# Kernel tuning notes

Hardware: AMD Instinct MI355X
Metric: run time of the kernel (lower is better)

The kernel has to match this reference:

```python
import jax, jax.numpy as jnp
import numpy as np

C = 8          # n_features
D = 256        # grid side
N = 1_000_000  # query points
K = 27         # kernel**3 neighborhood
OUTPUT_SCALE = 1.0


def _linear_params(key, fin, fout):
    kw, kb = jax.random.split(key)
    s = 1.0 / np.sqrt(fin)
    W = jax.random.uniform(kw, (fin, fout), jnp.float32, -s, s)
    b = jax.random.uniform(kb, (fout,), jnp.float32, -s, s)
    return W, b


def setup_inputs() -> dict:
    key = jax.random.key(0)
    ks = jax.random.split(key, 10)
    points = jax.random.uniform(ks[0], (N, 3), jnp.float32, 0.0, float(D - 1))
    grid = jax.random.normal(ks[1], (1, C, D, D, D), dtype=jnp.float32)
    Wc, bc = _linear_params(ks[2], K * C, C)
    W1, b1 = _linear_params(ks[3], 2 * C, 32)
    W2, b2 = _linear_params(ks[4], C + 32, 16)
    W3, b3 = _linear_params(ks[5], C + 16, 8)
    W4, b4 = _linear_params(ks[6], C + 8, C)
    Ws, bs = _linear_params(ks[7], C, 1)
    Wo, bo = _linear_params(ks[8], C, 1)
    return dict(points=points, grid=grid, Wc=Wc, bc=bc, W1=W1, b1=b1,
                W2=W2, b2=b2, W3=W3, b3=b3, W4=W4, b4=b4,
                Ws=Ws, bs=bs, Wo=Wo, bo=bo)


def _layernorm(z):
    # elementwise_affine=False, eps=1e-5, over last dim
    m = jnp.mean(z, axis=-1, keepdims=True)
    v = jnp.var(z, axis=-1, keepdims=True)
    return (z - m) * jax.lax.rsqrt(v + 1e-5)


def reference(points, grid, Wc, bc, W1, b1, W2, b2, W3, b3, W4, b4, Ws, bs, Wo, bo):
    act = jnp.tanh  # config.RENDERER.activation = torch.nn.Tanh()
    pad = 1  # kernel // 2
    # ReplicationPad3d on (1,C,D,H,W)
    g = jnp.pad(grid[0], ((0, 0), (pad, pad), (pad, pad), (pad, pad)), mode='edge')  # (C, D+2, D+2, D+2)
    pts = points + pad
    idx = jnp.floor(pts).astype(jnp.int32)  # (N,3)
    # 27-neighborhood offsets in loop order i,j,k in range(-1,2)
    r = jnp.arange(-1, 2)
    off = jnp.stack(jnp.meshgrid(r, r, r, indexing='ij'), axis=-1).reshape(K, 3)
    nb = idx[:, None, :] + off[None].astype(jnp.int32)  # (N,27,3)
    feat = g[:, nb[..., 0], nb[..., 1], nb[..., 2]]  # (C, N, 27)
    feat = jnp.transpose(feat, (1, 2, 0))            # (N, 27, C) point-major, neighbor, channel
    cen = g[:, idx[:, 0], idx[:, 1], idx[:, 2]].T    # (N, C)
    # use_count_renderer: normalize last channel (count) by global max
    max_count = jnp.maximum(jnp.max(feat[..., -1]), jnp.max(cen[:, -1])) + 1e-9
    feat = jnp.concatenate([feat[..., :-1], feat[..., -1:] / max_count], axis=-1)
    cen = jnp.concatenate([cen[:, :-1], cen[:, -1:] / max_count], axis=-1)
    x = feat.reshape(feat.shape[0], K * C)  # matches torch contiguous view (neighbor-then-channel)
    # DenseNet-style tiny MLP chain (Dropout2d is identity in eval)
    ctx = act(_layernorm(x @ Wc + bc))
    h = act(jnp.concatenate([cen, ctx], axis=1) @ W1 + b1)
    h = act(jnp.concatenate([cen, h], axis=1) @ W2 + b2)
    h = act(jnp.concatenate([cen, h], axis=1) @ W3 + b3)
    h = act(jnp.concatenate([cen, h], axis=1) @ W4 + b4)
    sdf = OUTPUT_SCALE * jnp.tanh(h @ Ws + bs)
    occ = jax.nn.sigmoid(h @ Wo + bo)
    return jnp.concatenate([sdf, occ], axis=1)  # (N, 2)
```

## Files before the change

kernel.cpp:

```cpp
#include <hip/hip_runtime.h>
#include <hip/hip_fp16.h>

typedef unsigned int u32;
typedef unsigned short u16;

__device__ __forceinline__ u32 encf(float f){ u32 u=__float_as_uint(f); return (u&0x80000000u)? ~u : (u|0x80000000u); }
__device__ __forceinline__ float decf(u32 u){ return (u&0x80000000u)? __uint_as_float(u&0x7fffffffu) : __uint_as_float(~u); }

__device__ __forceinline__ float fast_tanh(float x){
  x = fminf(fmaxf(x, -15.f), 15.f);
  float e = __expf(2.f*x);
  return (e - 1.f) * __builtin_amdgcn_rcpf(e + 1.f);
}
__device__ __forceinline__ float fast_sigmoid(float x){
  x = fminf(fmaxf(x, -15.f), 15.f);
  return __builtin_amdgcn_rcpf(1.f + __expf(-x));
}

__device__ __forceinline__ int base_ix(float p){
  return (int)floorf(p + 1.0f) - 1;
}

__global__ __launch_bounds__(256) void repack16(const float* __restrict__ g,
                                                uint4* __restrict__ rg,
                                                ushort4* __restrict__ zy4){
  u32 t = blockIdx.x*256u + threadIdx.x;
  u32 v0 = t << 2;
  const float4* gv = (const float4*)g;
  float4 C[8];
  #pragma unroll
  for (int c=0;c<8;c++) C[c] = gv[((u32)c<<22) + t];

  #pragma unroll
  for (int k=0;k<4;k++){
    float a[8];
    #pragma unroll
    for (int c=0;c<8;c++) a[c] = ((const float*)&C[c])[k];
    __half2 p0 = __floats2half2_rn(a[0],a[1]);
    __half2 p1 = __floats2half2_rn(a[2],a[3]);
    __half2 p2 = __floats2half2_rn(a[4],a[5]);
    __half2 p3 = __floats2half2_rn(a[6],a[7]);
    uint4 o;
    o.x=*(const u32*)&p0; o.y=*(const u32*)&p1; o.z=*(const u32*)&p2; o.w=*(const u32*)&p3;
    rg[v0+k]=o;
  }

  u32 z0 = v0 & 255u;
  u32 y  = (v0>>8) & 255u;
  const float* g7 = g + ((size_t)7u<<24);
  float zmax[4] = {-3.0e38f,-3.0e38f,-3.0e38f,-3.0e38f};
  #pragma unroll
  for (int r=0;r<3;r++){
    int yy = (int)y + r - 1;
    u32 ro = (yy<0 || yy>255)? v0 : (u32)((int)v0 + (r-1)*256);
    float4 f = (r==1)? C[7] : *(const float4*)(g7 + ro);
    float e0 = (z0==0u)?   f.x : g7[ro-1u];
    float e5 = (z0==252u)? f.w : g7[ro+4u];
    float e[6] = {e0, f.x, f.y, f.z, f.w, e5};
    #pragma unroll
    for (int k=0;k<4;k++)
      zmax[k] = fmaxf(zmax[k], fmaxf(e[k], fmaxf(e[k+1], e[k+2])));
  }
  ushort4 zo;
  zo.x = __half_as_ushort(__float2half_rn(zmax[0]));
  zo.y = __half_as_ushort(__float2half_rn(zmax[1]));
  zo.z = __half_as_ushort(__float2half_rn(zmax[2]));
  zo.w = __half_as_ushort(__float2half_rn(zmax[3]));
  zy4[t] = zo;
}

__device__ __forceinline__ u32 cell_id(int ix, int iy, int iz){
  return ((u32)(ix>>3)<<10) | ((u32)(iy>>3)<<5) | (u32)(iz>>3);
}

__global__ __launch_bounds__(256) void hist(const float* __restrict__ pts,
                                            u32* __restrict__ cnt, int n){
  for (int i = blockIdx.x*blockDim.x + threadIdx.x; i < n; i += gridDim.x*blockDim.x){
    int ix = base_ix(pts[3*i]);
    int iy = base_ix(pts[3*i+1]);
    int iz = base_ix(pts[3*i+2]);
    atomicAdd(&cnt[cell_id(ix,iy,iz)], 1u);
  }
}

__global__ __launch_bounds__(1024) void scan32k(const u32* __restrict__ cnt,
                                                u32* __restrict__ ofs){
  __shared__ u32 sums[1024];
  int t = threadIdx.x;
  u32 loc[32];
  u32 s = 0;
  #pragma unroll
  for (int k=0;k<32;k++){ loc[k] = cnt[t*32+k]; s += loc[k]; }
  sums[t] = s;
  __syncthreads();
  for (int off=1; off<1024; off<<=1){
    u32 v = (t>=off)? sums[t-off] : 0u;
    __syncthreads();
    sums[t] += v;
    __syncthreads();
  }
  u32 run = (t>0)? sums[t-1] : 0u;
  #pragma unroll
  for (int k=0;k<32;k++){ ofs[t*32+k] = run; run += loc[k]; }
}

__global__ __launch_bounds__(256) void scatter_max(const float* __restrict__ pts,
                                                   u32* __restrict__ ofs,
                                                   const u16* __restrict__ zy,
                                                   float4* __restrict__ srt,
                                                   u32* __restrict__ wmax, int n){
  __shared__ float red[4];
  float m = -3.0e38f;
  for (int i = blockIdx.x*blockDim.x + threadIdx.x; i < n; i += gridDim.x*blockDim.x){
    float px = pts[3*i], py = pts[3*i+1], pz = pts[3*i+2];
    int ix = base_ix(px), iy = base_ix(py), iz = base_ix(pz);
    u32 r = atomicAdd(&ofs[cell_id(ix,iy,iz)], 1u);
    srt[r] = make_float4(px, py, pz, __uint_as_float((u32)i));
    u32 cb = ((u32)ix<<16) | ((u32)iy<<8) | (u32)iz;
    u32 xm = (ix==0)? cb : cb - 65536u;
    float a = __half2float(__ushort_as_half(zy[xm]));
    float b = __half2float(__ushort_as_half(zy[cb]));
    float c = __half2float(__ushort_as_half(zy[cb + 65536u]));
    m = fmaxf(m, fmaxf(a, fmaxf(b, c)));
  }
  #pragma unroll
  for (int o=32;o>=1;o>>=1) m = fmaxf(m, __shfl_xor(m, o));
  int wid = threadIdx.x >> 6;
  if ((threadIdx.x & 63)==0) red[wid] = m;
  __syncthreads();
  if (threadIdx.x == 0){
    float r2 = fmaxf(fmaxf(red[0],red[1]), fmaxf(red[2],red[3]));
    atomicMax(wmax, encf(r2));
  }
}

__device__ __forceinline__ void mlp_tail(const float* __restrict__ cen,
                                         const float* __restrict__ acc0,
                                         float2* __restrict__ out, int i,
                                         const float* __restrict__ W1, const float* __restrict__ b1,
                                         const float* __restrict__ W2, const float* __restrict__ b2,
                                         const float* __restrict__ W3, const float* __restrict__ b3,
                                         const float* __restrict__ W4, const float* __restrict__ b4,
                                         const float* __restrict__ Ws, const float* __restrict__ bs,
                                         const float* __restrict__ Wo, const float* __restrict__ bo)
{
  float mean = 0.f;
  #pragma unroll
  for (int j=0;j<8;j++) mean += acc0[j];
  mean *= 0.125f;
  float var = 0.f;
  #pragma unroll
  for (int j=0;j<8;j++){ float t = acc0[j]-mean; var += t*t; }
  var *= 0.125f;
  float rs = rsqrtf(var + 1e-5f);
  float ctx[8];
  #pragma unroll
  for (int j=0;j<8;j++) ctx[j] = fast_tanh((acc0[j]-mean)*rs);

  float h1[32];
  #pragma unroll
  for (int j=0;j<32;j++){
    float s = b1[j];
    #pragma unroll
    for (int c=0;c<8;c++) s = fmaf(cen[c], W1[c*32 + j], s);
    #pragma unroll
    for (int c=0;c<8;c++) s = fmaf(ctx[c], W1[(8+c)*32 + j], s);
    h1[j] = fast_tanh(s);
  }
  float h2[16];
  #pragma unroll
  for (int j=0;j<16;j++){
    float s = b2[j];
    #pragma unroll
    for (int c=0;c<8;c++) s = fmaf(cen[c], W2[c*16 + j], s);
    #pragma unroll
    for (int c=0;c<32;c++) s = fmaf(h1[c], W2[(8+c)*16 + j], s);
    h2[j] = fast_tanh(s);
  }
  float h3[8];
  #pragma unroll
  for (int j=0;j<8;j++){
    float s = b3[j];
    #pragma unroll
    for (int c=0;c<8;c++) s = fmaf(cen[c], W3[c*8 + j], s);
    #pragma unroll
    for (int c=0;c<16;c++) s = fmaf(h2[c], W3[(8+c)*8 + j], s);
    h3[j] = fast_tanh(s);
  }
  float h4[8];
  #pragma unroll
  for (int j=0;j<8;j++){
    float s = b4[j];
    #pragma unroll
    for (int c=0;c<8;c++) s = fmaf(cen[c], W4[c*8 + j], s);
    #pragma unroll
    for (int c=0;c<8;c++) s = fmaf(h3[c], W4[(8+c)*8 + j], s);
    h4[j] = fast_tanh(s);
  }
  float ssdf = bs[0];
  float socc = bo[0];
  #pragma unroll
  for (int c=0;c<8;c++){
    ssdf = fmaf(h4[c], Ws[c], ssdf);
    socc = fmaf(h4[c], Wo[c], socc);
  }
  out[i] = make_float2(fast_tanh(ssdf), fast_sigmoid(socc));
}

__global__ __launch_bounds__(256,3) void kmain16(const float4* __restrict__ srt,
                                                 const uint4* __restrict__ rg,
                                                 const u32* __restrict__ wmax,
                                                 float2* __restrict__ out, int n,
                                                 const float* __restrict__ Wc, const float* __restrict__ bc,
                                                 const float* __restrict__ W1, const float* __restrict__ b1,
                                                 const float* __restrict__ W2, const float* __restrict__ b2,
                                                 const float* __restrict__ W3, const float* __restrict__ b3,
                                                 const float* __restrict__ W4, const float* __restrict__ b4,
                                                 const float* __restrict__ Ws, const float* __restrict__ bs,
                                                 const float* __restrict__ Wo, const float* __restrict__ bo)
{
  u32 nwg = gridDim.x;
  u32 qq = nwg >> 3, rr = nwg & 7u;
  u32 xcd = blockIdx.x & 7u, sub = blockIdx.x >> 3;
  u32 bid = (xcd < rr ? xcd*(qq+1u) : rr*(qq+1u) + (xcd-rr)*qq) + sub;

  int j = (int)(bid*256u + threadIdx.x);
  if (j >= n) return;
  float inv = 1.0f / (decf(*wmax) + 1e-9f);
  float4 rec = srt[j];
  int i = (int)__float_as_uint(rec.w);

  int ix = base_ix(rec.x);
  int iy = base_ix(rec.y);
  int iz = base_ix(rec.z);
  int xs[3] = {max(ix-1,0), ix, min(ix+1,255)};
  int ys[3] = {max(iy-1,0), iy, min(iy+1,255)};
  int zs[3] = {max(iz-1,0), iz, min(iz+1,255)};

  uint4 qv[27];
  #pragma unroll
  for (int a=0;a<3;a++)
  #pragma unroll
  for (int b=0;b<3;b++)
  #pragma unroll
  for (int d=0;d<3;d++)
    qv[(a*3+b)*3+d] = rg[((u32)xs[a]<<16) | ((u32)ys[b]<<8) | (u32)zs[d]];

  float cen[8];
  {
    uint4 qc = qv[13];
    float2 f0 = __half22float2(*(const __half2*)&qc.x);
    float2 f1 = __half22float2(*(const __half2*)&qc.y);
    float2 f2 = __half22float2(*(const __half2*)&qc.z);
    float2 f3 = __half22float2(*(const __half2*)&qc.w);
    cen[0]=f0.x; cen[1]=f0.y; cen[2]=f1.x; cen[3]=f1.y;
    cen[4]=f2.x; cen[5]=f2.y; cen[6]=f3.x; cen[7]=f3.y*inv;
  }

  float acc[8];
  #pragma unroll
  for (int jj=0;jj<8;jj++) acc[jj] = bc[jj];

  #pragma unroll
  for (int kk=0;kk<27;kk++){
    uint4 q2 = qv[kk];
    float2 f0 = __half22float2(*(const __half2*)&q2.x);
    float2 f1 = __half22float2(*(const __half2*)&q2.y);
    float2 f2 = __half22float2(*(const __half2*)&q2.z);
    float2 f3 = __half22float2(*(const __half2*)&q2.w);
    float v[8] = {f0.x,f0.y,f1.x,f1.y,f2.x,f2.y,f3.x, f3.y*inv};
    #pragma unroll
    for (int c=0;c<8;c++)
      #pragma unroll
      for (int jj=0;jj<8;jj++)
        acc[jj] = fmaf(v[c], Wc[(kk*8+c)*8 + jj], acc[jj]);
  }

  mlp_tail(cen, acc, out, i, W1,b1,W2,b2,W3,b3,W4,b4,Ws,bs,Wo,bo);
}

__global__ __launch_bounds__(256) void kmax_direct(const float* __restrict__ pts,
                                                   const float* __restrict__ g7,
                                                   u32* __restrict__ wmax, int n){
  float m = -3.0e38f;
  for (int i = blockIdx.x*blockDim.x + threadIdx.x; i < n; i += gridDim.x*blockDim.x){
    int ix = base_ix(pts[3*i]);
    int iy = base_ix(pts[3*i+1]);
    int iz = base_ix(pts[3*i+2]);
    int xs[3] = {max(ix-1,0), ix, min(ix+1,255)};
    int ys[3] = {max(iy-1,0), iy, min(iy+1,255)};
    int zs[3] = {max(iz-1,0), iz, min(iz+1,255)};
    #pragma unroll
    for (int a=0;a<3;a++)
    #pragma unroll
    for (int b=0;b<3;b++){
      u32 rb = ((u32)xs[a]<<16) | ((u32)ys[b]<<8);
      #pragma unroll
      for (int d=0;d<3;d++) m = fmaxf(m, g7[rb + (u32)zs[d]]);
    }
  }
  #pragma unroll
  for (int o=32;o>=1;o>>=1) m = fmaxf(m, __shfl_xor(m, o));
  if ((threadIdx.x & 63)==0) atomicMax(wmax, encf(m));
}

__global__ __launch_bounds__(256) void kmain_direct(const float* __restrict__ pts,
                                                    const float* __restrict__ g,
                                                    const u32* __restrict__ wmax,
                                                    float2* __restrict__ out, int n,
                                                    const float* __restrict__ Wc, const float* __restrict__ bc,
                                                    const float* __restrict__ W1, const float* __restrict__ b1,
                                                    const float* __restrict__ W2, const float* __restrict__ b2,
                                                    const float* __restrict__ W3, const float* __restrict__ b3,
                                                    const float* __restrict__ W4, const float* __restrict__ b4,
                                                    const float* __restrict__ Ws, const float* __restrict__ bs,
                                                    const float* __restrict__ Wo, const float* __restrict__ bo)
{
  int i = blockIdx.x*256 + threadIdx.x;
  if (i >= n) return;
  float inv = 1.0f / (decf(*wmax) + 1e-9f);

  int ix = base_ix(pts[3*i]);
  int iy = base_ix(pts[3*i+1]);
  int iz = base_ix(pts[3*i+2]);
  int xs[3] = {max(ix-1,0), ix, min(ix+1,255)};
  int ys[3] = {max(iy-1,0), iy, min(iy+1,255)};
  int zs[3] = {max(iz-1,0), iz, min(iz+1,255)};

  u32 cb = ((u32)ix<<16) | ((u32)iy<<8) | (u32)iz;
  float cen[8];
  #pragma unroll
  for (int c=0;c<8;c++) cen[c] = g[((u32)c<<24) + cb];
  cen[7] *= inv;

  float acc[8];
  #pragma unroll
  for (int j=0;j<8;j++) acc[j] = bc[j];

  #pragma unroll
  for (int a=0;a<3;a++)
  #pragma unroll
  for (int b=0;b<3;b++)
  #pragma unroll
  for (int d=0;d<3;d++){
    const int kk = (a*3+b)*3+d;
    u32 vb = ((u32)xs[a]<<16) | ((u32)ys[b]<<8) | (u32)zs[d];
    float v[8];
    #pragma unroll
    for (int c=0;c<8;c++) v[c] = g[((u32)c<<24) + vb];
    v[7] *= inv;
    #pragma unroll
    for (int c=0;c<8;c++)
      #pragma unroll
      for (int j=0;j<8;j++)
        acc[j] = fmaf(v[c], Wc[(kk*8+c)*8 + j], acc[j]);
  }

  mlp_tail(cen, acc, out, i, W1,b1,W2,b2,W3,b3,W4,b4,Ws,bs,Wo,bo);
}

extern "C" void kernel_launch(void* const* d_in, const int* in_sizes, int n_in,
                              void* d_out, int out_size, void* d_ws, size_t ws_size,
                              hipStream_t stream)
{
  const float* pts  = (const float*)d_in[0];
  const float* grid = (const float*)d_in[1];
  int n = in_sizes[0] / 3;

  const size_t NV       = (size_t)1 << 24;
  const size_t RG_BYTES = NV * 16;
  const size_t SL_BYTES = NV * 2;
  const size_t SRT_BYTES= (size_t)n * 16;
  const size_t CNT_BYTES= 32768 * 4;
  const size_t NEED     = RG_BYTES + SL_BYTES + SRT_BYTES + 2*CNT_BYTES + 64;

  if (ws_size >= NEED){
    char* base = (char*)d_ws;
    uint4*   rg   = (uint4*)base;
    u16*     zy   = (u16*)(base + RG_BYTES);
    float4*  srt  = (float4*)(base + RG_BYTES + SL_BYTES);
    u32*     cnt  = (u32*)(base + RG_BYTES + SL_BYTES + SRT_BYTES);
    u32*     ofs  = (u32*)(base + RG_BYTES + SL_BYTES + SRT_BYTES + CNT_BYTES);
    u32*     wmax = (u32*)(base + RG_BYTES + SL_BYTES + SRT_BYTES + 2*CNT_BYTES);

    hipMemsetAsync(cnt, 0, CNT_BYTES, stream);
    hipMemsetAsync(wmax, 0, 64, stream);
    repack16<<<16384, 256, 0, stream>>>(grid, rg, (ushort4*)zy);
    hist<<<2048, 256, 0, stream>>>(pts, cnt, n);
    scan32k<<<1, 1024, 0, stream>>>(cnt, ofs);
    scatter_max<<<2048, 256, 0, stream>>>(pts, ofs, zy, srt, wmax, n);
    kmain16<<<(n+255)/256, 256, 0, stream>>>(srt, rg, wmax, (float2*)d_out, n,
        (const float*)d_in[2],  (const float*)d_in[3],
        (const float*)d_in[4],  (const float*)d_in[5],
        (const float*)d_in[6],  (const float*)d_in[7],
        (const float*)d_in[8],  (const float*)d_in[9],
        (const float*)d_in[10], (const float*)d_in[11],
        (const float*)d_in[12], (const float*)d_in[13],
        (const float*)d_in[14], (const float*)d_in[15]);
  } else {
    u32* wmax = (u32*)d_ws;
    hipMemsetAsync(wmax, 0, 64, stream);
    kmax_direct<<<2048, 256, 0, stream>>>(pts, grid + ((size_t)7<<24), wmax, n);
    kmain_direct<<<(n+255)/256, 256, 0, stream>>>(pts, grid, wmax, (float2*)d_out, n,
        (const float*)d_in[2],  (const float*)d_in[3],
        (const float*)d_in[4],  (const float*)d_in[5],
        (const float*)d_in[6],  (const float*)d_in[7],
        (const float*)d_in[8],  (const float*)d_in[9],
        (const float*)d_in[10], (const float*)d_in[11],
        (const float*)d_in[12], (const float*)d_in[13],
        (const float*)d_in[14], (const float*)d_in[15]);
  }
}
```

Measured before the change: 504.3 us.

## Use packed fp16 dot2 for context conv and MLP with prepacked half weights

Adds a small kernel that packs all MLP weights into fp16 pairs, folding the count normalization into the Wc weights for the last channel. The main kernel then does the 27-neighbor context layer and every MLP layer with v_dot2 fp16 instructions that accumulate in fp32, which removes the half-to-float conversions and halves the FMA count. Activations are re-packed to fp16 between layers. This trades some precision, from fp16 weights and activations and the clamped scaled weight, for less ALU work.

```diff
diff --git a/kernel.cpp b/kernel.cpp
--- a/kernel.cpp
+++ b/kernel.cpp
@@ -3,6 +3,7 @@
 
 typedef unsigned int u32;
 typedef unsigned short u16;
+typedef _Float16 half2_t __attribute__((ext_vector_type(2)));
 
 __device__ __forceinline__ u32 encf(float f){ u32 u=__float_as_uint(f); return (u&0x80000000u)? ~u : (u|0x80000000u); }
 __device__ __forceinline__ float decf(u32 u){ return (u&0x80000000u)? __uint_as_float(u&0x7fffffffu) : __uint_as_float(~u); }
@@ -19,6 +20,14 @@
 
 __device__ __forceinline__ int base_ix(float p){
   return (int)floorf(p + 1.0f) - 1;
+}
+
+__device__ __forceinline__ half2_t h2cast(u32 u){ return __builtin_bit_cast(half2_t, u); }
+__device__ __forceinline__ half2_t pk(float a, float b){
+  return __builtin_bit_cast(half2_t, __builtin_amdgcn_cvt_pkrtz(a, b));
+}
+__device__ __forceinline__ float dot2(half2_t a, half2_t b, float c){
+  return __builtin_amdgcn_fdot2(a, b, c, false);
 }
 
 __global__ __launch_bounds__(256) void repack16(const float* __restrict__ g,
@@ -134,90 +143,59 @@
   }
 }
 
-__device__ __forceinline__ void mlp_tail(const float* __restrict__ cen,
-                                         const float* __restrict__ acc0,
-                                         float2* __restrict__ out, int i,
-                                         const float* __restrict__ W1, const float* __restrict__ b1,
-                                         const float* __restrict__ W2, const float* __restrict__ b2,
-                                         const float* __restrict__ W3, const float* __restrict__ b3,
-                                         const float* __restrict__ W4, const float* __restrict__ b4,
-                                         const float* __restrict__ Ws, const float* __restrict__ bs,
-                                         const float* __restrict__ Wo, const float* __restrict__ bo)
-{
-  float mean = 0.f;
-  #pragma unroll
-  for (int j=0;j<8;j++) mean += acc0[j];
-  mean *= 0.125f;
-  float var = 0.f;
-  #pragma unroll
-  for (int j=0;j<8;j++){ float t = acc0[j]-mean; var += t*t; }
-  var *= 0.125f;
-  float rs = rsqrtf(var + 1e-5f);
-  float ctx[8];
-  #pragma unroll
-  for (int j=0;j<8;j++) ctx[j] = fast_tanh((acc0[j]-mean)*rs);
-
-  float h1[32];
-  #pragma unroll
-  for (int j=0;j<32;j++){
-    float s = b1[j];
-    #pragma unroll
-    for (int c=0;c<8;c++) s = fmaf(cen[c], W1[c*32 + j], s);
-    #pragma unroll
-    for (int c=0;c<8;c++) s = fmaf(ctx[c], W1[(8+c)*32 + j], s);
-    h1[j] = fast_tanh(s);
-  }
-  float h2[16];
-  #pragma unroll
-  for (int j=0;j<16;j++){
-    float s = b2[j];
-    #pragma unroll
-    for (int c=0;c<8;c++) s = fmaf(cen[c], W2[c*16 + j], s);
-    #pragma unroll
-    for (int c=0;c<32;c++) s = fmaf(h1[c], W2[(8+c)*16 + j], s);
-    h2[j] = fast_tanh(s);
-  }
-  float h3[8];
-  #pragma unroll
-  for (int j=0;j<8;j++){
-    float s = b3[j];
-    #pragma unroll
-    for (int c=0;c<8;c++) s = fmaf(cen[c], W3[c*8 + j], s);
-    #pragma unroll
-    for (int c=0;c<16;c++) s = fmaf(h2[c], W3[(8+c)*8 + j], s);
-    h3[j] = fast_tanh(s);
-  }
-  float h4[8];
-  #pragma unroll
-  for (int j=0;j<8;j++){
-    float s = b4[j];
-    #pragma unroll
-    for (int c=0;c<8;c++) s = fmaf(cen[c], W4[c*8 + j], s);
-    #pragma unroll
-    for (int c=0;c<8;c++) s = fmaf(h3[c], W4[(8+c)*8 + j], s);
-    h4[j] = fast_tanh(s);
-  }
-  float ssdf = bs[0];
-  float socc = bo[0];
-  #pragma unroll
-  for (int c=0;c<8;c++){
-    ssdf = fmaf(h4[c], Ws[c], ssdf);
-    socc = fmaf(h4[c], Wo[c], socc);
-  }
-  out[i] = make_float2(fast_tanh(ssdf), fast_sigmoid(socc));
+__global__ __launch_bounds__(256) void packw(const float* __restrict__ Wc,
+                                             const float* __restrict__ W1,
+                                             const float* __restrict__ W2,
+                                             const float* __restrict__ W3,
+                                             const float* __restrict__ W4,
+                                             const float* __restrict__ Ws,
+                                             const float* __restrict__ Wo,
+                                             const u32* __restrict__ wmax,
+                                             u32* __restrict__ dst){
+  int t = blockIdx.x*256 + threadIdx.x;
+  if (t >= 1608) return;
+  float inv = 1.0f / (decf(*wmax) + 1e-9f);
+  float w0, w1;
+  if (t < 864){
+    int j = t & 7, p = (t>>3) & 3, kk = t>>5;
+    w0 = Wc[(kk*8 + 2*p)*8 + j];
+    w1 = Wc[(kk*8 + 2*p+1)*8 + j];
+    if (p == 3){
+      w1 = fminf(fmaxf(w1*inv, -60000.f), 60000.f);
+    }
+  } else if (t < 1120){
+    int u = t - 864; int j = u & 31, p = u >> 5;
+    w0 = W1[(2*p)*32 + j]; w1 = W1[(2*p+1)*32 + j];
+  } else if (t < 1440){
+    int u = t - 1120; int j = u & 15, p = u >> 4;
+    w0 = W2[(2*p)*16 + j]; w1 = W2[(2*p+1)*16 + j];
+  } else if (t < 1536){
+    int u = t - 1440; int j = u & 7, p = u >> 3;
+    w0 = W3[(2*p)*8 + j]; w1 = W3[(2*p+1)*8 + j];
+  } else if (t < 1600){
+    int u = t - 1536; int j = u & 7, p = u >> 3;
+    w0 = W4[(2*p)*8 + j]; w1 = W4[(2*p+1)*8 + j];
+  } else if (t < 1604){
+    int p = t - 1600; w0 = Ws[2*p]; w1 = Ws[2*p+1];
+  } else {
+    int p = t - 1604; w0 = Wo[2*p]; w1 = Wo[2*p+1];
+  }
+  __half2 h = __floats2half2_rn(w0, w1);
+  dst[t] = *(const u32*)&h;
 }
 
 __global__ __launch_bounds__(256,3) void kmain16(const float4* __restrict__ srt,
                                                  const uint4* __restrict__ rg,
                                                  const u32* __restrict__ wmax,
+                                                 const u32* __restrict__ wpk,
                                                  float2* __restrict__ out, int n,
-                                                 const float* __restrict__ Wc, const float* __restrict__ bc,
-                                                 const float* __restrict__ W1, const float* __restrict__ b1,
-                                                 const float* __restrict__ W2, const float* __restrict__ b2,
-                                                 const float* __restrict__ W3, const float* __restrict__ b3,
-                                                 const float* __restrict__ W4, const float* __restrict__ b4,
-                                                 const float* __restrict__ Ws, const float* __restrict__ bs,
-                                                 const float* __restrict__ Wo, const float* __restrict__ bo)
+                                                 const float* __restrict__ bc,
+                                                 const float* __restrict__ b1,
+                                                 const float* __restrict__ b2,
+                                                 const float* __restrict__ b3,
+                                                 const float* __restrict__ b4,
+                                                 const float* __restrict__ bs,
+                                                 const float* __restrict__ bo)
 {
   u32 nwg = gridDim.x;
   u32 qq = nwg >> 3, rr = nwg & 7u;
@@ -245,6 +223,28 @@
   #pragma unroll
   for (int d=0;d<3;d++)
     qv[(a*3+b)*3+d] = rg[((u32)xs[a]<<16) | ((u32)ys[b]<<8) | (u32)zs[d]];
+
+  float acc[8];
+  #pragma unroll
+  for (int jj=0;jj<8;jj++) acc[jj] = bc[jj];
+
+  #pragma unroll
+  for (int kk=0;kk<27;kk++){
+    half2_t v0 = h2cast(qv[kk].x);
+    half2_t v1 = h2cast(qv[kk].y);
+    half2_t v2 = h2cast(qv[kk].z);
+    half2_t v3 = h2cast(qv[kk].w);
+    const u32* w = wpk + kk*32;
+    #pragma unroll
+    for (int jj=0;jj<8;jj++){
+      float s = acc[jj];
+      s = dot2(v0, h2cast(w[jj]),      s);
+      s = dot2(v1, h2cast(w[8+jj]),   s);
+      s = dot2(v2, h2cast(w[16+jj]),  s);
+      s = dot2(v3, h2cast(w[24+jj]),  s);
+      acc[jj] = s;
+    }
+  }
 
   float cen[8];
   {
@@ -257,26 +257,169 @@
     cen[4]=f2.x; cen[5]=f2.y; cen[6]=f3.x; cen[7]=f3.y*inv;
   }
 
-  float acc[8];
-  #pragma unroll
-  for (int jj=0;jj<8;jj++) acc[jj] = bc[jj];
-
-  #pragma unroll
-  for (int kk=0;kk<27;kk++){
-    uint4 q2 = qv[kk];
-    float2 f0 = __half22float2(*(const __half2*)&q2.x);
-    float2 f1 = __half22float2(*(const __half2*)&q2.y);
-    float2 f2 = __half22float2(*(const __half2*)&q2.z);
-    float2 f3 = __half22float2(*(const __half2*)&q2.w);
-    float v[8] = {f0.x,f0.y,f1.x,f1.y,f2.x,f2.y,f3.x, f3.y*inv};
-    #pragma unroll
-    for (int c=0;c<8;c++)
-      #pragma unroll
-      for (int jj=0;jj<8;jj++)
-        acc[jj] = fmaf(v[c], Wc[(kk*8+c)*8 + jj], acc[jj]);
-  }
-
-  mlp_tail(cen, acc, out, i, W1,b1,W2,b2,W3,b3,W4,b4,Ws,bs,Wo,bo);
+  float mean = 0.f;
+  #pragma unroll
+  for (int jj=0;jj<8;jj++) mean += acc[jj];
+  mean *= 0.125f;
+  float var = 0.f;
+  #pragma unroll
+  for (int jj=0;jj<8;jj++){ float d = acc[jj]-mean; var += d*d; }
+  var *= 0.125f;
+  float rs = rsqrtf(var + 1e-5f);
+
+  half2_t cenp[4], ctxp[4];
+  #pragma unroll
+  for (int p=0;p<4;p++){
+    cenp[p] = pk(cen[2*p], cen[2*p+1]);
+    ctxp[p] = pk(fast_tanh((acc[2*p]-mean)*rs), fast_tanh((acc[2*p+1]-mean)*rs));
+  }
+
+  const u32* W1h = wpk + 864;
+  const u32* W2h = wpk + 1120;
+  const u32* W3h = wpk + 1440;
+  const u32* W4h = wpk + 1536;
+
+  half2_t h1p[16];
+  #pragma unroll
+  for (int p2=0;p2<16;p2++){
+    float s0 = b1[2*p2], s1 = b1[2*p2+1];
+    #pragma unroll
+    for (int p=0;p<4;p++){
+      s0 = dot2(cenp[p], h2cast(W1h[p*32 + 2*p2]),     s0);
+      s1 = dot2(cenp[p], h2cast(W1h[p*32 + 2*p2+1]),   s1);
+      s0 = dot2(ctxp[p], h2cast(W1h[(4+p)*32 + 2*p2]), s0);
+      s1 = dot2(ctxp[p], h2cast(W1h[(4+p)*32 + 2*p2+1]), s1);
+    }
+    h1p[p2] = pk(fast_tanh(s0), fast_tanh(s1));
+  }
+
+  half2_t h2p[8];
+  #pragma unroll
+  for (int p2=0;p2<8;p2++){
+    float s0 = b2[2*p2], s1 = b2[2*p2+1];
+    #pragma unroll
+    for (int p=0;p<4;p++){
+      s0 = dot2(cenp[p], h2cast(W2h[p*16 + 2*p2]),   s0);
+      s1 = dot2(cenp[p], h2cast(W2h[p*16 + 2*p2+1]), s1);
+    }
+    #pragma unroll
+    for (int p=0;p<16;p++){
+      s0 = dot2(h1p[p], h2cast(W2h[(4+p)*16 + 2*p2]),   s0);
+      s1 = dot2(h1p[p], h2cast(W2h[(4+p)*16 + 2*p2+1]), s1);
+    }
+    h2p[p2] = pk(fast_tanh(s0), fast_tanh(s1));
+  }
+
+  half2_t h3p[4];
+  #pragma unroll
+  for (int p2=0;p2<4;p2++){
+    float s0 = b3[2*p2], s1 = b3[2*p2+1];
+    #pragma unroll
+    for (int p=0;p<4;p++){
+      s0 = dot2(cenp[p], h2cast(W3h[p*8 + 2*p2]),   s0);
+      s1 = dot2(cenp[p], h2cast(W3h[p*8 + 2*p2+1]), s1);
+    }
+    #pragma unroll
+    for (int p=0;p<8;p++){
+      s0 = dot2(h2p[p], h2cast(W3h[(4+p)*8 + 2*p2]),   s0);
+      s1 = dot2(h2p[p], h2cast(W3h[(4+p)*8 + 2*p2+1]), s1);
+    }
+    h3p[p2] = pk(fast_tanh(s0), fast_tanh(s1));
+  }
+
+  half2_t h4p[4];
+  #pragma unroll
+  for (int p2=0;p2<4;p2++){
+    float s0 = b4[2*p2], s1 = b4[2*p2+1];
+    #pragma unroll
+    for (int p=0;p<4;p++){
+      s0 = dot2(cenp[p], h2cast(W4h[p*8 + 2*p2]),   s0);
+      s1 = dot2(cenp[p], h2cast(W4h[p*8 + 2*p2+1]), s1);
+      s0 = dot2(h3p[p], h2cast(W4h[(4+p)*8 + 2*p2]),   s0);
+      s1 = dot2(h3p[p], h2cast(W4h[(4+p)*8 + 2*p2+1]), s1);
+    }
+    h4p[p2] = pk(fast_tanh(s0), fast_tanh(s1));
+  }
+
+  float ssdf = bs[0], socc = bo[0];
+  #pragma unroll
+  for (int p=0;p<4;p++){
+    ssdf = dot2(h4p[p], h2cast(wpk[1600+p]), ssdf);
+    socc = dot2(h4p[p], h2cast(wpk[1604+p]), socc);
+  }
+  out[i] = make_float2(fast_tanh(ssdf), fast_sigmoid(socc));
+}
+
+__device__ __forceinline__ void mlp_tail_f32(const float* __restrict__ cen,
+                                             const float* __restrict__ acc0,
+                                             float2* __restrict__ out, int i,
+                                             const float* __restrict__ W1, const float* __restrict__ b1,
+                                             const float* __restrict__ W2, const float* __restrict__ b2,
+                                             const float* __restrict__ W3, const float* __restrict__ b3,
+                                             const float* __restrict__ W4, const float* __restrict__ b4,
+                                             const float* __restrict__ Ws, const float* __restrict__ bs,
+                                             const float* __restrict__ Wo, const float* __restrict__ bo)
+{
+  float mean = 0.f;
+  #pragma unroll
+  for (int j=0;j<8;j++) mean += acc0[j];
+  mean *= 0.125f;
+  float var = 0.f;
+  #pragma unroll
+  for (int j=0;j<8;j++){ float t = acc0[j]-mean; var += t*t; }
+  var *= 0.125f;
+  float rs = rsqrtf(var + 1e-5f);
+  float ctx[8];
+  #pragma unroll
+  for (int j=0;j<8;j++) ctx[j] = fast_tanh((acc0[j]-mean)*rs);
+  float h1[32];
+  #pragma unroll
+  for (int j=0;j<32;j++){
+    float s = b1[j];
+    #pragma unroll
+    for (int c=0;c<8;c++) s = fmaf(cen[c], W1[c*32 + j], s);
+    #pragma unroll
+    for (int c=0;c<8;c++) s = fmaf(ctx[c], W1[(8+c)*32 + j], s);
+    h1[j] = fast_tanh(s);
+  }
+  float h2[16];
+  #pragma unroll
+  for (int j=0;j<16;j++){
+    float s = b2[j];
+    #pragma unroll
+    for (int c=0;c<8;c++) s = fmaf(cen[c], W2[c*16 + j], s);
+    #pragma unroll
+    for (int c=0;c<32;c++) s = fmaf(h1[c], W2[(8+c)*16 + j], s);
+    h2[j] = fast_tanh(s);
+  }
+  float h3[8];
+  #pragma unroll
+  for (int j=0;j<8;j++){
+    float s = b3[j];
+    #pragma unroll
+    for (int c=0;c<8;c++) s = fmaf(cen[c], W3[c*8 + j], s);
+    #pragma unroll
+    for (int c=0;c<16;c++) s = fmaf(h2[c], W3[(8+c)*8 + j], s);
+    h3[j] = fast_tanh(s);
+  }
+  float h4[8];
+  #pragma unroll
+  for (int j=0;j<8;j++){
+    float s = b4[j];
+    #pragma unroll
+    for (int c=0;c<8;c++) s = fmaf(cen[c], W4[c*8 + j], s);
+    #pragma unroll
+    for (int c=0;c<8;c++) s = fmaf(h3[c], W4[(8+c)*8 + j], s);
+    h4[j] = fast_tanh(s);
+  }
+  float ssdf = bs[0];
+  float socc = bo[0];
+  #pragma unroll
+  for (int c=0;c<8;c++){
+    ssdf = fmaf(h4[c], Ws[c], ssdf);
+    socc = fmaf(h4[c], Wo[c], socc);
+  }
+  out[i] = make_float2(fast_tanh(ssdf), fast_sigmoid(socc));
 }
 
 __global__ __launch_bounds__(256) void kmax_direct(const float* __restrict__ pts,
@@ -319,24 +462,20 @@
   int i = blockIdx.x*256 + threadIdx.x;
   if (i >= n) return;
   float inv = 1.0f / (decf(*wmax) + 1e-9f);
-
   int ix = base_ix(pts[3*i]);
   int iy = base_ix(pts[3*i+1]);
   int iz = base_ix(pts[3*i+2]);
   int xs[3] = {max(ix-1,0), ix, min(ix+1,255)};
   int ys[3] = {max(iy-1,0), iy, min(iy+1,255)};
   int zs[3] = {max(iz-1,0), iz, min(iz+1,255)};
-
   u32 cb = ((u32)ix<<16) | ((u32)iy<<8) | (u32)iz;
   float cen[8];
   #pragma unroll
   for (int c=0;c<8;c++) cen[c] = g[((u32)c<<24) + cb];
   cen[7] *= inv;
-
   float acc[8];
   #pragma unroll
   for (int j=0;j<8;j++) acc[j] = bc[j];
-
   #pragma unroll
   for (int a=0;a<3;a++)
   #pragma unroll
@@ -355,8 +494,7 @@
       for (int j=0;j<8;j++)
         acc[j] = fmaf(v[c], Wc[(kk*8+c)*8 + j], acc[j]);
   }
-
-  mlp_tail(cen, acc, out, i, W1,b1,W2,b2,W3,b3,W4,b4,Ws,bs,Wo,bo);
+  mlp_tail_f32(cen, acc, out, i, W1,b1,W2,b2,W3,b3,W4,b4,Ws,bs,Wo,bo);
 }
 
 extern "C" void kernel_launch(void* const* d_in, const int* in_sizes, int n_in,
@@ -372,7 +510,8 @@
   const size_t SL_BYTES = NV * 2;
   const size_t SRT_BYTES= (size_t)n * 16;
   const size_t CNT_BYTES= 32768 * 4;
-  const size_t NEED     = RG_BYTES + SL_BYTES + SRT_BYTES + 2*CNT_BYTES + 64;
+  const size_t PK_BYTES = 8192;
+  const size_t NEED     = RG_BYTES + SL_BYTES + SRT_BYTES + 2*CNT_BYTES + 64 + PK_BYTES;
 
   if (ws_size >= NEED){
     char* base = (char*)d_ws;
@@ -382,6 +521,7 @@
     u32*     cnt  = (u32*)(base + RG_BYTES + SL_BYTES + SRT_BYTES);
     u32*     ofs  = (u32*)(base + RG_BYTES + SL_BYTES + SRT_BYTES + CNT_BYTES);
     u32*     wmax = (u32*)(base + RG_BYTES + SL_BYTES + SRT_BYTES + 2*CNT_BYTES);
+    u32*     wpk  = (u32*)(base + RG_BYTES + SL_BYTES + SRT_BYTES + 2*CNT_BYTES + 64);
 
     hipMemsetAsync(cnt, 0, CNT_BYTES, stream);
     hipMemsetAsync(wmax, 0, 64, stream);
@@ -389,14 +529,15 @@
     hist<<<2048, 256, 0, stream>>>(pts, cnt, n);
     scan32k<<<1, 1024, 0, stream>>>(cnt, ofs);
     scatter_max<<<2048, 256, 0, stream>>>(pts, ofs, zy, srt, wmax, n);
-    kmain16<<<(n+255)/256, 256, 0, stream>>>(srt, rg, wmax, (float2*)d_out, n,
-        (const float*)d_in[2],  (const float*)d_in[3],
-        (const float*)d_in[4],  (const float*)d_in[5],
-        (const float*)d_in[6],  (const float*)d_in[7],
-        (const float*)d_in[8],  (const float*)d_in[9],
-        (const float*)d_in[10], (const float*)d_in[11],
-        (const float*)d_in[12], (const float*)d_in[13],
-        (const float*)d_in[14], (const float*)d_in[15]);
+    packw<<<7, 256, 0, stream>>>((const float*)d_in[2], (const float*)d_in[4],
+                                 (const float*)d_in[6], (const float*)d_in[8],
+                                 (const float*)d_in[10], (const float*)d_in[12],
+                                 (const float*)d_in[14], wmax, wpk);
+    kmain16<<<(n+255)/256, 256, 0, stream>>>(srt, rg, wmax, wpk, (float2*)d_out, n,
+        (const float*)d_in[3],  (const float*)d_in[5],
+        (const float*)d_in[7],  (const float*)d_in[9],
+        (const float*)d_in[11], (const float*)d_in[13],
+        (const float*)d_in[15]);
   } else {
     u32* wmax = (u32*)d_ws;
     hipMemsetAsync(wmax, 0, 64, stream);
```

Result: faster. 485.4 us (-3.8%).
